# Optimization experiments

Hardware: AMD Instinct MI355X
Metric: run time of the kernel (lower is better)

## Reference

```python
import jax, jax.numpy as jnp
import numpy as np

N = 2_097_152  # total atoms
G = 32_768     # number of graphs (~64 atoms each)
EPS = 1e-4     # sign-detection threshold from the original code


def setup_inputs() -> dict:
    key = jax.random.key(0)
    k1, k2 = jax.random.split(key)
    pos = jax.random.normal(k1, (N, 3), dtype=jnp.float32) * 3.0
    batch = jnp.sort(jax.random.randint(k2, (N,), 0, G))
    return {"pos": pos, "batch": batch, "num_graphs": G}


def reference(pos, batch, num_graphs):
    n = pos.shape[0]
    dtype = pos.dtype

    # per-graph centroid (scatter_mean)
    counts = jax.ops.segment_sum(jnp.ones((n,), dtype), batch, num_segments=num_graphs)
    center = jax.ops.segment_sum(pos, batch, num_segments=num_graphs) / jnp.maximum(counts, 1.0)[:, None]
    pc = pos - center[batch]                      # [N,3] centered positions

    # per-atom inertia contribution: r^2 * I - p p^T, then scatter_add per graph
    r_sq = jnp.sum(pc * pc, axis=-1)              # [N]
    outer = jnp.einsum('ni,nj->nij', pc, pc)      # [N,3,3]
    I_atom = r_sq[:, None, None] * jnp.eye(3, dtype=dtype) - outer
    I_mol = jax.ops.segment_sum(I_atom, batch, num_segments=num_graphs)  # [G,3,3]

    L, Q = jnp.linalg.eigh(I_mol)                 # Q: [G,3,3], columns = principal axes

    # projections of centered positions onto the (pre-flip) eigenbasis.
    # NOTE: in the torch loop, p_proj is computed once before any sign flips, and
    # flipping column 0 does not affect p_proj[:,1], so axes 0 and 1 are independent.
    proj = jnp.einsum('ni,nij->nj', pc, Q[batch])  # [N,3]

    idx = jnp.arange(n)

    def axis_sign(a):
        # parallel "first atom (in original order) with |proj| > EPS" per graph
        qual = jnp.abs(proj[:, a]) > EPS
        key_idx = jnp.where(qual, idx, n)
        first = jax.ops.segment_min(key_idx, batch, num_segments=num_graphs)  # [G]
        found = first < n
        val = proj[jnp.minimum(first, n - 1), a]
        return jnp.where(found & (val < 0), -1.0, 1.0).astype(dtype)

    s0 = axis_sign(0)
    s1 = axis_sign(1)
    q0 = Q[:, :, 0] * s0[:, None]
    q1 = Q[:, :, 1] * s1[:, None]
    q2 = jnp.cross(q0, q1)  # enforce right-handed frame
    return jnp.stack([q0, q1, q2], axis=-1)       # [G,3,3]
```

## Files before the change

### kernel.cpp

```cpp
#include <hip/hip_runtime.h>
#include <math.h>

#define CANON_EPS 1e-4f

__device__ __forceinline__ void jacobi3_f32(float a00, float a11, float a22,
                                            float a01, float a02, float a12,
                                            float Q[3][3]) {
  float A00 = a00, A11 = a11, A22 = a22;
  float A01 = a01, A02 = a02, A12 = a12;
  float Q00 = 1.f, Q01 = 0.f, Q02 = 0.f;
  float Q10 = 0.f, Q11 = 1.f, Q12 = 0.f;
  float Q20 = 0.f, Q21 = 0.f, Q22 = 1.f;

#define ROT(App, Aqq, Apq, Akp, Akq, Qrp0, Qrq0, Qrp1, Qrq1, Qrp2, Qrq2)     \
  {                                                                          \
    float apq = Apq;                                                         \
    float theta = (Aqq - App) / (2.0f * apq);                                \
    float t = copysignf(1.0f, theta) /                                       \
              (fabsf(theta) + sqrtf(1.0f + theta * theta));                  \
    t = (apq == 0.0f) ? 0.0f : t;                    \
    float c = 1.0f / sqrtf(1.0f + t * t);                                    \
    float s = t * c;                                                         \
    App = App - t * apq;                                                     \
    Aqq = Aqq + t * apq;                                                     \
    Apq = 0.0f;                                                              \
    float akp = Akp, akq = Akq;                                              \
    Akp = c * akp - s * akq;                                                 \
    Akq = s * akp + c * akq;                                                 \
    float r0p = Qrp0, r0q = Qrq0;                                            \
    Qrp0 = c * r0p - s * r0q;                                                \
    Qrq0 = s * r0p + c * r0q;                                                \
    float r1p = Qrp1, r1q = Qrq1;                                            \
    Qrp1 = c * r1p - s * r1q;                                                \
    Qrq1 = s * r1p + c * r1q;                                                \
    float r2p = Qrp2, r2q = Qrq2;                                            \
    Qrp2 = c * r2p - s * r2q;                                                \
    Qrq2 = s * r2p + c * r2q;                                                \
  }

#pragma unroll
  for (int sweep = 0; sweep < 4; ++sweep) {
    ROT(A00, A11, A01, A02, A12, Q00, Q01, Q10, Q11, Q20, Q21);
    ROT(A00, A22, A02, A01, A12, Q00, Q02, Q10, Q12, Q20, Q22);
    ROT(A11, A22, A12, A01, A02, Q01, Q02, Q11, Q12, Q21, Q22);
  }
#undef ROT

  float w0 = A00, w1 = A11, w2 = A22;
#define CSWAP(wa, wb, qa0, qb0, qa1, qb1, qa2, qb2)                          \
  {                                                                          \
    bool sw = (wb) < (wa);                                                   \
    float tw = wa; wa = sw ? wb : wa; wb = sw ? tw : wb;                     \
    float t0 = qa0; qa0 = sw ? qb0 : qa0; qb0 = sw ? t0 : qb0;               \
    float t1 = qa1; qa1 = sw ? qb1 : qa1; qb1 = sw ? t1 : qb1;               \
    float t2 = qa2; qa2 = sw ? qb2 : qa2; qb2 = sw ? t2 : qb2;               \
  }
  CSWAP(w0, w1, Q00, Q01, Q10, Q11, Q20, Q21);
  CSWAP(w1, w2, Q01, Q02, Q11, Q12, Q21, Q22);
  CSWAP(w0, w1, Q00, Q01, Q10, Q11, Q20, Q21);
#undef CSWAP

  Q[0][0] = Q00; Q[0][1] = Q01; Q[0][2] = Q02;
  Q[1][0] = Q10; Q[1][1] = Q11; Q[1][2] = Q12;
  Q[2][0] = Q20; Q[2][1] = Q21; Q[2][2] = Q22;
}

__global__ __launch_bounds__(256) void canon_all_kernel(
    const float* __restrict__ pos, const int* __restrict__ batch,
    float* __restrict__ out, int n, int G) {
  __shared__ float lmom[16][9];
  __shared__ float latm[16][12];
  __shared__ int lsc[16][2];

  int tid = (int)threadIdx.x;
  int lg = tid >> 4;
  int sub = tid & 15;
  int lane = tid & 63;
  int gid = (int)blockIdx.x * 16 + lg;
  bool gv = gid < G;

  int t0 = gv ? gid : (G - 1);
  int half = (lane >> 3) & 1;
  int tgt = t0 + half;
  int j = lane & 7;
  int base = lane & 0x30;

  int r = 1;
  while (r < n) r <<= 3;
  int lo0 = 0, lo1 = 0;
  while (r > 1) {
    int step = r >> 3;
    int myLo = half ? lo1 : lo0;
    int m = myLo + j * step;
    int mm = m - 1;
    mm = mm < 0 ? 0 : (mm > n - 1 ? n - 1 : mm);
    bool c = (j == 0) || ((m <= n) && (batch[mm] < tgt));
    unsigned long long b = __ballot(c);
    unsigned c0 = (unsigned)((b >> base) & 0xFEull);
    unsigned c1 = (unsigned)((b >> (base + 8)) & 0xFEull);
    lo0 += __popc(c0) * step;
    lo1 += __popc(c1) * step;
    r = step;
  }
  {
    int i0 = lo0 < n - 1 ? lo0 : n - 1;
    int i1 = lo1 < n - 1 ? lo1 : n - 1;
    lo0 += ((lo0 < n) && (batch[i0] < t0)) ? 1 : 0;
    lo1 += ((lo1 < n) && (batch[i1] < t0 + 1)) ? 1 : 0;
  }
  int s = lo0, e = lo1;
  int cnt = e - s;

  float sx = 0.f, sy = 0.f, sz = 0.f;
  float sxx = 0.f, syy = 0.f, szz = 0.f, sxy = 0.f, sxz = 0.f, syz = 0.f;
  float r0x = 0.f, r0y = 0.f, r0z = 0.f;

#pragma unroll
  for (int k = 0; k < 5; ++k) {
    int i = s + sub + 16 * k;
    bool in = i < e;
    int ii = in ? i : 0;
    float rx = pos[3 * ii + 0];
    float ry = pos[3 * ii + 1];
    float rz = pos[3 * ii + 2];
    if (k == 0) { r0x = rx; r0y = ry; r0z = rz; }
    float m = in ? 1.0f : 0.0f;
    float x = rx * m, y = ry * m, z = rz * m;
    sx += x; sy += y; sz += z;
    sxx = fmaf(x, x, sxx); syy = fmaf(y, y, syy); szz = fmaf(z, z, szz);
    sxy = fmaf(x, y, sxy); sxz = fmaf(x, z, sxz); syz = fmaf(y, z, syz);
  }
  for (int i = s + 80 + sub; i < e; i += 16) {
    float x = pos[3 * i + 0];
    float y = pos[3 * i + 1];
    float z = pos[3 * i + 2];
    sx += x; sy += y; sz += z;
    sxx = fmaf(x, x, sxx); syy = fmaf(y, y, syy); szz = fmaf(z, z, szz);
    sxy = fmaf(x, y, sxy); sxz = fmaf(x, z, sxz); syz = fmaf(y, z, syz);
  }

#define RED16(v)                                                             \
  v += __shfl_xor(v, 1); v += __shfl_xor(v, 2);                              \
  v += __shfl_xor(v, 4); v += __shfl_xor(v, 8);
  RED16(sx) RED16(sy) RED16(sz)
  RED16(sxx) RED16(syy) RED16(szz)
  RED16(sxy) RED16(sxz) RED16(syz)
#undef RED16

  if (sub < 4 && gv) {
    latm[lg][3 * sub + 0] = r0x;
    latm[lg][3 * sub + 1] = r0y;
    latm[lg][3 * sub + 2] = r0z;
  }
  if (sub == 0 && gv) {
    float fn = (float)(cnt > 0 ? cnt : 1);
    float inv = 1.0f / fn;
    float mx = sx * inv, my = sy * inv, mz = sz * inv;
    float Sxx = fmaf(-fn * mx, mx, sxx);
    float Syy = fmaf(-fn * my, my, syy);
    float Szz = fmaf(-fn * mz, mz, szz);
    float Sxy = fmaf(-fn * mx, my, sxy);
    float Sxz = fmaf(-fn * mx, mz, sxz);
    float Syz = fmaf(-fn * my, mz, syz);
    lmom[lg][0] = mx; lmom[lg][1] = my; lmom[lg][2] = mz;
    lmom[lg][3] = Syy + Szz;
    lmom[lg][4] = Sxx + Szz;
    lmom[lg][5] = Sxx + Syy;
    lmom[lg][6] = -Sxy;
    lmom[lg][7] = -Sxz;
    lmom[lg][8] = -Syz;
    lsc[lg][0] = s; lsc[lg][1] = cnt;
  }
  __syncthreads();

  if (tid < 16) {
    int g = (int)blockIdx.x * 16 + tid;
    if (g < G) {
      float cx = lmom[tid][0], cy = lmom[tid][1], cz = lmom[tid][2];
      float Q[3][3];
      jacobi3_f32(lmom[tid][3], lmom[tid][4], lmom[tid][5], lmom[tid][6],
                  lmom[tid][7], lmom[tid][8], Q);

      float q00 = Q[0][0], q10 = Q[1][0], q20 = Q[2][0];
      float q01 = Q[0][1], q11 = Q[1][1], q21 = Q[2][1];

      int s2 = lsc[tid][0];
      int cnt2 = lsc[tid][1];

      bool found0 = false, found1 = false;
      float v0s = 0.f, v1s = 0.f;
#define CHECK(J)                                                             \
  if ((J) < cnt2) {                                                          \
    float x = latm[tid][3 * (J) + 0] - cx;                                   \
    float y = latm[tid][3 * (J) + 1] - cy;                                   \
    float z = latm[tid][3 * (J) + 2] - cz;                                   \
    float p0 = x * q00 + y * q10 + z * q20;                                  \
    float p1 = x * q01 + y * q11 + z * q21;                                  \
    if (!found0 && fabsf(p0) > CANON_EPS) { v0s = p0; found0 = true; }       \
    if (!found1 && fabsf(p1) > CANON_EPS) { v1s = p1; found1 = true; }       \
  }
      CHECK(0) CHECK(1) CHECK(2) CHECK(3)
#undef CHECK
      for (int i = s2 + 4; i < s2 + cnt2 && !(found0 && found1); ++i) {
        float x = pos[3 * i + 0] - cx;
        float y = pos[3 * i + 1] - cy;
        float z = pos[3 * i + 2] - cz;
        float p0 = x * q00 + y * q10 + z * q20;
        float p1 = x * q01 + y * q11 + z * q21;
        if (!found0 && fabsf(p0) > CANON_EPS) { v0s = p0; found0 = true; }
        if (!found1 && fabsf(p1) > CANON_EPS) { v1s = p1; found1 = true; }
      }
      float s0 = (found0 && v0s < 0.f) ? -1.f : 1.f;
      float s1 = (found1 && v1s < 0.f) ? -1.f : 1.f;

      float q0x = q00 * s0, q0y = q10 * s0, q0z = q20 * s0;
      float q1x = q01 * s1, q1y = q11 * s1, q1z = q21 * s1;
      float q2x = q0y * q1z - q0z * q1y;
      float q2y = q0z * q1x - q0x * q1z;
      float q2z = q0x * q1y - q0y * q1x;
      float* o = out + (size_t)g * 9;
      o[0] = q0x; o[1] = q1x; o[2] = q2x;
      o[3] = q0y; o[4] = q1y; o[5] = q2y;
      o[6] = q0z; o[7] = q1z; o[8] = q2z;
    }
  }
}

extern "C" void kernel_launch(void* const* d_in, const int* in_sizes, int n_in,
                              void* d_out, int out_size, void* d_ws, size_t ws_size,
                              hipStream_t stream) {
  const float* pos = (const float*)d_in[0];
  const int* batch = (const int*)d_in[1];
  float* out = (float*)d_out;

  int n = in_sizes[0] / 3;
  int G = out_size / 9;

  canon_all_kernel<<<(G + 15) / 16, 256, 0, stream>>>(pos, batch, out, n, G);
}
```

Before: 21.10 us.

## Stage block's contiguous atom positions in LDS with float4 loads

```diff
diff --git a/kernel.cpp b/kernel.cpp
--- a/kernel.cpp
+++ b/kernel.cpp
@@ -2,6 +2,7 @@
 #include <math.h>
 
 #define CANON_EPS 1e-4f
+#define MAX_STAGE 1536
 
 __device__ __forceinline__ void jacobi3_f32(float a00, float a11, float a22,
                                             float a01, float a02, float a12,
@@ -68,6 +69,7 @@
 __global__ __launch_bounds__(256) void canon_all_kernel(
     const float* __restrict__ pos, const int* __restrict__ batch,
     float* __restrict__ out, int n, int G) {
+  __shared__ float spos[MAX_STAGE * 3 + 8];
   __shared__ float lmom[16][9];
   __shared__ float latm[16][12];
   __shared__ int lsc[16][2];
@@ -111,32 +113,76 @@
   int s = lo0, e = lo1;
   int cnt = e - s;
 
+  if (sub == 0) { lsc[lg][0] = s; lsc[lg][1] = cnt; }
+  __syncthreads();
+
+  int lastLg = G - 1 - (int)blockIdx.x * 16;
+  lastLg = lastLg > 15 ? 15 : lastLg;
+  int sB = lsc[0][0];
+  int eB = lsc[lastLg][0] + lsc[lastLg][1];
+  int range = eB - sB;
+  bool useLds = (range <= MAX_STAGE);
+
+  int d0 = (3 * sB) & ~3;
+  if (useLds) {
+    int numd = 3 * eB - d0;
+    for (int d4 = tid * 4; d4 < numd; d4 += 256 * 4) {
+      int gd = d0 + d4;
+      if (gd + 4 <= 3 * n) {
+        float4 v = *reinterpret_cast<const float4*>(pos + gd);
+        spos[d4 + 0] = v.x; spos[d4 + 1] = v.y;
+        spos[d4 + 2] = v.z; spos[d4 + 3] = v.w;
+      } else {
+        for (int q = 0; q < 4; ++q)
+          if (gd + q < 3 * n) spos[d4 + q] = pos[gd + q];
+      }
+    }
+  }
+  __syncthreads();
+
   float sx = 0.f, sy = 0.f, sz = 0.f;
   float sxx = 0.f, syy = 0.f, szz = 0.f, sxy = 0.f, sxz = 0.f, syz = 0.f;
-  float r0x = 0.f, r0y = 0.f, r0z = 0.f;
-
+
+  if (useLds) {
+    for (int i = s + sub; i < e; i += 16) {
+      int dd = 3 * i - d0;
+      float x = spos[dd + 0];
+      float y = spos[dd + 1];
+      float z = spos[dd + 2];
+      sx += x; sy += y; sz += z;
+      sxx = fmaf(x, x, sxx); syy = fmaf(y, y, syy); szz = fmaf(z, z, szz);
+      sxy = fmaf(x, y, sxy); sxz = fmaf(x, z, sxz); syz = fmaf(y, z, syz);
+    }
+  } else {
+    float r0x = 0.f, r0y = 0.f, r0z = 0.f;
 #pragma unroll
-  for (int k = 0; k < 5; ++k) {
-    int i = s + sub + 16 * k;
-    bool in = i < e;
-    int ii = in ? i : 0;
-    float rx = pos[3 * ii + 0];
-    float ry = pos[3 * ii + 1];
-    float rz = pos[3 * ii + 2];
-    if (k == 0) { r0x = rx; r0y = ry; r0z = rz; }
-    float m = in ? 1.0f : 0.0f;
-    float x = rx * m, y = ry * m, z = rz * m;
-    sx += x; sy += y; sz += z;
-    sxx = fmaf(x, x, sxx); syy = fmaf(y, y, syy); szz = fmaf(z, z, szz);
-    sxy = fmaf(x, y, sxy); sxz = fmaf(x, z, sxz); syz = fmaf(y, z, syz);
-  }
-  for (int i = s + 80 + sub; i < e; i += 16) {
-    float x = pos[3 * i + 0];
-    float y = pos[3 * i + 1];
-    float z = pos[3 * i + 2];
-    sx += x; sy += y; sz += z;
-    sxx = fmaf(x, x, sxx); syy = fmaf(y, y, syy); szz = fmaf(z, z, szz);
-    sxy = fmaf(x, y, sxy); sxz = fmaf(x, z, sxz); syz = fmaf(y, z, syz);
+    for (int k = 0; k < 5; ++k) {
+      int i = s + sub + 16 * k;
+      bool in = i < e;
+      int ii = in ? i : 0;
+      float rx = pos[3 * ii + 0];
+      float ry = pos[3 * ii + 1];
+      float rz = pos[3 * ii + 2];
+      if (k == 0) { r0x = rx; r0y = ry; r0z = rz; }
+      float m = in ? 1.0f : 0.0f;
+      float x = rx * m, y = ry * m, z = rz * m;
+      sx += x; sy += y; sz += z;
+      sxx = fmaf(x, x, sxx); syy = fmaf(y, y, syy); szz = fmaf(z, z, szz);
+      sxy = fmaf(x, y, sxy); sxz = fmaf(x, z, sxz); syz = fmaf(y, z, syz);
+    }
+    for (int i = s + 80 + sub; i < e; i += 16) {
+      float x = pos[3 * i + 0];
+      float y = pos[3 * i + 1];
+      float z = pos[3 * i + 2];
+      sx += x; sy += y; sz += z;
+      sxx = fmaf(x, x, sxx); syy = fmaf(y, y, syy); szz = fmaf(z, z, szz);
+      sxy = fmaf(x, y, sxy); sxz = fmaf(x, z, sxz); syz = fmaf(y, z, syz);
+    }
+    if (sub < 4 && gv) {
+      latm[lg][3 * sub + 0] = r0x;
+      latm[lg][3 * sub + 1] = r0y;
+      latm[lg][3 * sub + 2] = r0z;
+    }
   }
 
 #define RED16(v)                                                             \
@@ -147,11 +193,6 @@
   RED16(sxy) RED16(sxz) RED16(syz)
 #undef RED16
 
-  if (sub < 4 && gv) {
-    latm[lg][3 * sub + 0] = r0x;
-    latm[lg][3 * sub + 1] = r0y;
-    latm[lg][3 * sub + 2] = r0z;
-  }
   if (sub == 0 && gv) {
     float fn = (float)(cnt > 0 ? cnt : 1);
     float inv = 1.0f / fn;
@@ -169,7 +210,6 @@
     lmom[lg][6] = -Sxy;
     lmom[lg][7] = -Sxz;
     lmom[lg][8] = -Syz;
-    lsc[lg][0] = s; lsc[lg][1] = cnt;
   }
   __syncthreads();
 
@@ -189,6 +229,18 @@
 
       bool found0 = false, found1 = false;
       float v0s = 0.f, v1s = 0.f;
+      if (useLds) {
+        for (int k = 0; k < cnt2 && !(found0 && found1); ++k) {
+          int dd = 3 * (s2 + k) - d0;
+          float x = spos[dd + 0] - cx;
+          float y = spos[dd + 1] - cy;
+          float z = spos[dd + 2] - cz;
+          float p0 = x * q00 + y * q10 + z * q20;
+          float p1 = x * q01 + y * q11 + z * q21;
+          if (!found0 && fabsf(p0) > CANON_EPS) { v0s = p0; found0 = true; }
+          if (!found1 && fabsf(p1) > CANON_EPS) { v1s = p1; found1 = true; }
+        }
+      } else {
 #define CHECK(J)                                                             \
   if ((J) < cnt2) {                                                          \
     float x = latm[tid][3 * (J) + 0] - cx;                                   \
@@ -199,16 +251,17 @@
     if (!found0 && fabsf(p0) > CANON_EPS) { v0s = p0; found0 = true; }       \
     if (!found1 && fabsf(p1) > CANON_EPS) { v1s = p1; found1 = true; }       \
   }
-      CHECK(0) CHECK(1) CHECK(2) CHECK(3)
+        CHECK(0) CHECK(1) CHECK(2) CHECK(3)
 #undef CHECK
-      for (int i = s2 + 4; i < s2 + cnt2 && !(found0 && found1); ++i) {
-        float x = pos[3 * i + 0] - cx;
-        float y = pos[3 * i + 1] - cy;
-        float z = pos[3 * i + 2] - cz;
-        float p0 = x * q00 + y * q10 + z * q20;
-        float p1 = x * q01 + y * q11 + z * q21;
-        if (!found0 && fabsf(p0) > CANON_EPS) { v0s = p0; found0 = true; }
-        if (!found1 && fabsf(p1) > CANON_EPS) { v1s = p1; found1 = true; }
+        for (int i = s2 + 4; i < s2 + cnt2 && !(found0 && found1); ++i) {
+          float x = pos[3 * i + 0] - cx;
+          float y = pos[3 * i + 1] - cy;
+          float z = pos[3 * i + 2] - cz;
+          float p0 = x * q00 + y * q10 + z * q20;
+          float p1 = x * q01 + y * q11 + z * q21;
+          if (!found0 && fabsf(p0) > CANON_EPS) { v0s = p0; found0 = true; }
+          if (!found1 && fabsf(p1) > CANON_EPS) { v1s = p1; found1 = true; }
+        }
       }
       float s0 = (found0 && v0s < 0.f) ? -1.f : 1.f;
       float s1 = (found1 && v1s < 0.f) ? -1.f : 1.f;
```

After: 24.12 us. 1.14x slower.

## Run eigen-solve redundantly per 16-lane group and find sign atom via ballot

Applied to the files above, without the earlier changes.

```diff
diff --git a/kernel.cpp b/kernel.cpp
--- a/kernel.cpp
+++ b/kernel.cpp
@@ -2,81 +2,14 @@
 #include <math.h>
 
 #define CANON_EPS 1e-4f
-
-__device__ __forceinline__ void jacobi3_f32(float a00, float a11, float a22,
-                                            float a01, float a02, float a12,
-                                            float Q[3][3]) {
-  float A00 = a00, A11 = a11, A22 = a22;
-  float A01 = a01, A02 = a02, A12 = a12;
-  float Q00 = 1.f, Q01 = 0.f, Q02 = 0.f;
-  float Q10 = 0.f, Q11 = 1.f, Q12 = 0.f;
-  float Q20 = 0.f, Q21 = 0.f, Q22 = 1.f;
-
-#define ROT(App, Aqq, Apq, Akp, Akq, Qrp0, Qrq0, Qrp1, Qrq1, Qrp2, Qrq2)     \
-  {                                                                          \
-    float apq = Apq;                                                         \
-    float theta = (Aqq - App) / (2.0f * apq);                                \
-    float t = copysignf(1.0f, theta) /                                       \
-              (fabsf(theta) + sqrtf(1.0f + theta * theta));                  \
-    t = (apq == 0.0f) ? 0.0f : t;                    \
-    float c = 1.0f / sqrtf(1.0f + t * t);                                    \
-    float s = t * c;                                                         \
-    App = App - t * apq;                                                     \
-    Aqq = Aqq + t * apq;                                                     \
-    Apq = 0.0f;                                                              \
-    float akp = Akp, akq = Akq;                                              \
-    Akp = c * akp - s * akq;                                                 \
-    Akq = s * akp + c * akq;                                                 \
-    float r0p = Qrp0, r0q = Qrq0;                                            \
-    Qrp0 = c * r0p - s * r0q;                                                \
-    Qrq0 = s * r0p + c * r0q;                                                \
-    float r1p = Qrp1, r1q = Qrq1;                                            \
-    Qrp1 = c * r1p - s * r1q;                                                \
-    Qrq1 = s * r1p + c * r1q;                                                \
-    float r2p = Qrp2, r2q = Qrq2;                                            \
-    Qrp2 = c * r2p - s * r2q;                                                \
-    Qrq2 = s * r2p + c * r2q;                                                \
-  }
-
-#pragma unroll
-  for (int sweep = 0; sweep < 4; ++sweep) {
-    ROT(A00, A11, A01, A02, A12, Q00, Q01, Q10, Q11, Q20, Q21);
-    ROT(A00, A22, A02, A01, A12, Q00, Q02, Q10, Q12, Q20, Q22);
-    ROT(A11, A22, A12, A01, A02, Q01, Q02, Q11, Q12, Q21, Q22);
-  }
-#undef ROT
-
-  float w0 = A00, w1 = A11, w2 = A22;
-#define CSWAP(wa, wb, qa0, qb0, qa1, qb1, qa2, qb2)                          \
-  {                                                                          \
-    bool sw = (wb) < (wa);                                                   \
-    float tw = wa; wa = sw ? wb : wa; wb = sw ? tw : wb;                     \
-    float t0 = qa0; qa0 = sw ? qb0 : qa0; qb0 = sw ? t0 : qb0;               \
-    float t1 = qa1; qa1 = sw ? qb1 : qa1; qb1 = sw ? t1 : qb1;               \
-    float t2 = qa2; qa2 = sw ? qb2 : qa2; qb2 = sw ? t2 : qb2;               \
-  }
-  CSWAP(w0, w1, Q00, Q01, Q10, Q11, Q20, Q21);
-  CSWAP(w1, w2, Q01, Q02, Q11, Q12, Q21, Q22);
-  CSWAP(w0, w1, Q00, Q01, Q10, Q11, Q20, Q21);
-#undef CSWAP
-
-  Q[0][0] = Q00; Q[0][1] = Q01; Q[0][2] = Q02;
-  Q[1][0] = Q10; Q[1][1] = Q11; Q[1][2] = Q12;
-  Q[2][0] = Q20; Q[2][1] = Q21; Q[2][2] = Q22;
-}
 
 __global__ __launch_bounds__(256) void canon_all_kernel(
     const float* __restrict__ pos, const int* __restrict__ batch,
     float* __restrict__ out, int n, int G) {
-  __shared__ float lmom[16][9];
-  __shared__ float latm[16][12];
-  __shared__ int lsc[16][2];
-
   int tid = (int)threadIdx.x;
-  int lg = tid >> 4;
   int sub = tid & 15;
   int lane = tid & 63;
-  int gid = (int)blockIdx.x * 16 + lg;
+  int gid = ((int)blockIdx.x * 256 + tid) >> 4;
   bool gv = gid < G;
 
   int t0 = gv ? gid : (G - 1);
@@ -111,9 +44,9 @@
   int s = lo0, e = lo1;
   int cnt = e - s;
 
+  float ax[5], ay[5], az[5];
   float sx = 0.f, sy = 0.f, sz = 0.f;
   float sxx = 0.f, syy = 0.f, szz = 0.f, sxy = 0.f, sxz = 0.f, syz = 0.f;
-  float r0x = 0.f, r0y = 0.f, r0z = 0.f;
 
 #pragma unroll
   for (int k = 0; k < 5; ++k) {
@@ -123,7 +56,7 @@
     float rx = pos[3 * ii + 0];
     float ry = pos[3 * ii + 1];
     float rz = pos[3 * ii + 2];
-    if (k == 0) { r0x = rx; r0y = ry; r0z = rz; }
+    ax[k] = rx; ay[k] = ry; az[k] = rz;
     float m = in ? 1.0f : 0.0f;
     float x = rx * m, y = ry * m, z = rz * m;
     sx += x; sy += y; sz += z;
@@ -147,82 +80,136 @@
   RED16(sxy) RED16(sxz) RED16(syz)
 #undef RED16
 
-  if (sub < 4 && gv) {
-    latm[lg][3 * sub + 0] = r0x;
-    latm[lg][3 * sub + 1] = r0y;
-    latm[lg][3 * sub + 2] = r0z;
-  }
-  if (sub == 0 && gv) {
-    float fn = (float)(cnt > 0 ? cnt : 1);
-    float inv = 1.0f / fn;
-    float mx = sx * inv, my = sy * inv, mz = sz * inv;
-    float Sxx = fmaf(-fn * mx, mx, sxx);
-    float Syy = fmaf(-fn * my, my, syy);
-    float Szz = fmaf(-fn * mz, mz, szz);
-    float Sxy = fmaf(-fn * mx, my, sxy);
-    float Sxz = fmaf(-fn * mx, mz, sxz);
-    float Syz = fmaf(-fn * my, mz, syz);
-    lmom[lg][0] = mx; lmom[lg][1] = my; lmom[lg][2] = mz;
-    lmom[lg][3] = Syy + Szz;
-    lmom[lg][4] = Sxx + Szz;
-    lmom[lg][5] = Sxx + Syy;
-    lmom[lg][6] = -Sxy;
-    lmom[lg][7] = -Sxz;
-    lmom[lg][8] = -Syz;
-    lsc[lg][0] = s; lsc[lg][1] = cnt;
-  }
-  __syncthreads();
-
-  if (tid < 16) {
-    int g = (int)blockIdx.x * 16 + tid;
-    if (g < G) {
-      float cx = lmom[tid][0], cy = lmom[tid][1], cz = lmom[tid][2];
-      float Q[3][3];
-      jacobi3_f32(lmom[tid][3], lmom[tid][4], lmom[tid][5], lmom[tid][6],
-                  lmom[tid][7], lmom[tid][8], Q);
-
-      float q00 = Q[0][0], q10 = Q[1][0], q20 = Q[2][0];
-      float q01 = Q[0][1], q11 = Q[1][1], q21 = Q[2][1];
-
-      int s2 = lsc[tid][0];
-      int cnt2 = lsc[tid][1];
-
-      bool found0 = false, found1 = false;
-      float v0s = 0.f, v1s = 0.f;
-#define CHECK(J)                                                             \
-  if ((J) < cnt2) {                                                          \
-    float x = latm[tid][3 * (J) + 0] - cx;                                   \
-    float y = latm[tid][3 * (J) + 1] - cy;                                   \
-    float z = latm[tid][3 * (J) + 2] - cz;                                   \
-    float p0 = x * q00 + y * q10 + z * q20;                                  \
-    float p1 = x * q01 + y * q11 + z * q21;                                  \
-    if (!found0 && fabsf(p0) > CANON_EPS) { v0s = p0; found0 = true; }       \
-    if (!found1 && fabsf(p1) > CANON_EPS) { v1s = p1; found1 = true; }       \
-  }
-      CHECK(0) CHECK(1) CHECK(2) CHECK(3)
-#undef CHECK
-      for (int i = s2 + 4; i < s2 + cnt2 && !(found0 && found1); ++i) {
-        float x = pos[3 * i + 0] - cx;
-        float y = pos[3 * i + 1] - cy;
-        float z = pos[3 * i + 2] - cz;
-        float p0 = x * q00 + y * q10 + z * q20;
-        float p1 = x * q01 + y * q11 + z * q21;
-        if (!found0 && fabsf(p0) > CANON_EPS) { v0s = p0; found0 = true; }
-        if (!found1 && fabsf(p1) > CANON_EPS) { v1s = p1; found1 = true; }
-      }
-      float s0 = (found0 && v0s < 0.f) ? -1.f : 1.f;
-      float s1 = (found1 && v1s < 0.f) ? -1.f : 1.f;
-
-      float q0x = q00 * s0, q0y = q10 * s0, q0z = q20 * s0;
-      float q1x = q01 * s1, q1y = q11 * s1, q1z = q21 * s1;
-      float q2x = q0y * q1z - q0z * q1y;
-      float q2y = q0z * q1x - q0x * q1z;
-      float q2z = q0x * q1y - q0y * q1x;
-      float* o = out + (size_t)g * 9;
-      o[0] = q0x; o[1] = q1x; o[2] = q2x;
-      o[3] = q0y; o[4] = q1y; o[5] = q2y;
-      o[6] = q0z; o[7] = q1z; o[8] = q2z;
-    }
+  float fn = (float)(cnt > 0 ? cnt : 1);
+  float inv = 1.0f / fn;
+  float cx = sx * inv, cy = sy * inv, cz = sz * inv;
+  float Sxx = fmaf(-fn * cx, cx, sxx);
+  float Syy = fmaf(-fn * cy, cy, syy);
+  float Szz = fmaf(-fn * cz, cz, szz);
+  float Sxy = fmaf(-fn * cx, cy, sxy);
+  float Sxz = fmaf(-fn * cx, cz, sxz);
+  float Syz = fmaf(-fn * cy, cz, syz);
+
+  float A00 = Syy + Szz, A11 = Sxx + Szz, A22 = Sxx + Syy;
+  float A01 = -Sxy, A02 = -Sxz, A12 = -Syz;
+  float Q00 = 1.f, Q01 = 0.f, Q02 = 0.f;
+  float Q10 = 0.f, Q11 = 1.f, Q12 = 0.f;
+  float Q20 = 0.f, Q21 = 0.f, Q22 = 1.f;
+
+#define ROT(App, Aqq, Apq, Akp, Akq, Qrp0, Qrq0, Qrp1, Qrq1, Qrp2, Qrq2)     \
+  {                                                                          \
+    float apq = Apq;                                                         \
+    float theta = (Aqq - App) / (2.0f * apq);                                \
+    float t = copysignf(1.0f, theta) /                                       \
+              (fabsf(theta) + sqrtf(1.0f + theta * theta));                  \
+    t = (apq == 0.0f) ? 0.0f : t;                    \
+    float c = 1.0f / sqrtf(1.0f + t * t);                                    \
+    float s_ = t * c;                                                        \
+    App = App - t * apq;                                                     \
+    Aqq = Aqq + t * apq;                                                     \
+    Apq = 0.0f;                                                              \
+    float akp = Akp, akq = Akq;                                              \
+    Akp = c * akp - s_ * akq;                                                \
+    Akq = s_ * akp + c * akq;                                                \
+    float r0p = Qrp0, r0q = Qrq0;                                            \
+    Qrp0 = c * r0p - s_ * r0q;                                               \
+    Qrq0 = s_ * r0p + c * r0q;                                               \
+    float r1p = Qrp1, r1q = Qrq1;                                            \
+    Qrp1 = c * r1p - s_ * r1q;                                               \
+    Qrq1 = s_ * r1p + c * r1q;                                               \
+    float r2p = Qrp2, r2q = Qrq2;                                            \
+    Qrp2 = c * r2p - s_ * r2q;                                               \
+    Qrq2 = s_ * r2p + c * r2q;                                               \
+  }
+#pragma unroll
+  for (int sweep = 0; sweep < 4; ++sweep) {
+    ROT(A00, A11, A01, A02, A12, Q00, Q01, Q10, Q11, Q20, Q21);
+    ROT(A00, A22, A02, A01, A12, Q00, Q02, Q10, Q12, Q20, Q22);
+    ROT(A11, A22, A12, A01, A02, Q01, Q02, Q11, Q12, Q21, Q22);
+  }
+#undef ROT
+
+  float w0 = A00, w1 = A11, w2 = A22;
+#define CSWAP(wa, wb, qa0, qb0, qa1, qb1, qa2, qb2)                          \
+  {                                                                          \
+    bool sw = (wb) < (wa);                                                   \
+    float tw = wa; wa = sw ? wb : wa; wb = sw ? tw : wb;                     \
+    float u0 = qa0; qa0 = sw ? qb0 : qa0; qb0 = sw ? u0 : qb0;               \
+    float u1 = qa1; qa1 = sw ? qb1 : qa1; qb1 = sw ? u1 : qb1;               \
+    float u2 = qa2; qa2 = sw ? qb2 : qa2; qb2 = sw ? u2 : qb2;               \
+  }
+  CSWAP(w0, w1, Q00, Q01, Q10, Q11, Q20, Q21);
+  CSWAP(w1, w2, Q01, Q02, Q11, Q12, Q21, Q22);
+  CSWAP(w0, w1, Q00, Q01, Q10, Q11, Q20, Q21);
+#undef CSWAP
+
+  bool found0 = false, found1 = false;
+  float v0s = 0.f, v1s = 0.f;
+#pragma unroll
+  for (int k = 0; k < 5; ++k) {
+    bool in = (s + sub + 16 * k) < e;
+    float x = ax[k] - cx, y = ay[k] - cy, z = az[k] - cz;
+    float p0 = x * Q00 + y * Q10 + z * Q20;
+    float p1 = x * Q01 + y * Q11 + z * Q21;
+    unsigned long long b0 = __ballot(in && (fabsf(p0) > CANON_EPS));
+    unsigned long long b1 = __ballot(in && (fabsf(p1) > CANON_EPS));
+    unsigned m0 = (unsigned)((b0 >> base) & 0xFFFFull);
+    unsigned m1 = (unsigned)((b1 >> base) & 0xFFFFull);
+    if (!found0 && m0) {
+      int l = __ffs(m0) - 1;
+      v0s = __shfl(p0, base + l);
+      found0 = true;
+    }
+    if (!found1 && m1) {
+      int l = __ffs(m1) - 1;
+      v1s = __shfl(p1, base + l);
+      found1 = true;
+    }
+  }
+  for (int bb = s + 80; bb < e && !(found0 && found1); bb += 16) {
+    int i = bb + sub;
+    bool in = i < e;
+    int ii = in ? i : 0;
+    float x = pos[3 * ii + 0] - cx;
+    float y = pos[3 * ii + 1] - cy;
+    float z = pos[3 * ii + 2] - cz;
+    float p0 = x * Q00 + y * Q10 + z * Q20;
+    float p1 = x * Q01 + y * Q11 + z * Q21;
+    unsigned long long b0 = __ballot(in && (fabsf(p0) > CANON_EPS));
+    unsigned long long b1 = __ballot(in && (fabsf(p1) > CANON_EPS));
+    unsigned m0 = (unsigned)((b0 >> base) & 0xFFFFull);
+    unsigned m1 = (unsigned)((b1 >> base) & 0xFFFFull);
+    if (!found0 && m0) {
+      int l = __ffs(m0) - 1;
+      v0s = __shfl(p0, base + l);
+      found0 = true;
+    }
+    if (!found1 && m1) {
+      int l = __ffs(m1) - 1;
+      v1s = __shfl(p1, base + l);
+      found1 = true;
+    }
+  }
+  float s0 = (found0 && v0s < 0.f) ? -1.f : 1.f;
+  float s1 = (found1 && v1s < 0.f) ? -1.f : 1.f;
+
+  float q0x = Q00 * s0, q0y = Q10 * s0, q0z = Q20 * s0;
+  float q1x = Q01 * s1, q1y = Q11 * s1, q1z = Q21 * s1;
+  float q2x = q0y * q1z - q0z * q1y;
+  float q2y = q0z * q1x - q0x * q1z;
+  float q2z = q0x * q1y - q0y * q1x;
+
+  if (gv && sub < 9) {
+    float v = q0x;
+    v = (sub == 1) ? q1x : v;
+    v = (sub == 2) ? q2x : v;
+    v = (sub == 3) ? q0y : v;
+    v = (sub == 4) ? q1y : v;
+    v = (sub == 5) ? q2y : v;
+    v = (sub == 6) ? q0z : v;
+    v = (sub == 7) ? q1z : v;
+    v = (sub == 8) ? q2z : v;
+    out[(size_t)gid * 9 + sub] = v;
   }
 }
 
```

After: 29.80 us. 41.2% more time.
